# Optimization experiments

Hardware: AMD Instinct MI355X
Metric: run time of the kernel (lower is better)

## Reference

```python
import jax, jax.numpy as jnp
import numpy as np

DIM = 1024
HEADS = 16
HEAD_DIM = DIM // HEADS
EPS = 1e-5


def layer_norm(x, w, b):
    # normalize over last dim (head_dim)
    mu = jnp.mean(x, axis=-1, keepdims=True)
    var = jnp.mean(jnp.square(x - mu), axis=-1, keepdims=True)
    return (x - mu) * jax.lax.rsqrt(var + EPS) * w + b


def setup_inputs() -> dict:
    key = jax.random.key(0)
    ks = jax.random.split(key, 8)
    B, N = 2, 2048
    x = jax.random.normal(ks[0], (B, N, DIM), dtype=jnp.float32)
    mask = jax.random.randint(ks[1], (B, 1, N, N), 0, 2) == 1  # True = masked out
    qkv_w = jax.random.normal(ks[2], (3 * DIM, DIM), dtype=jnp.float32) * (DIM ** -0.5)
    q_norm_w = jnp.ones((HEAD_DIM,), dtype=jnp.float32)
    q_norm_b = jnp.zeros((HEAD_DIM,), dtype=jnp.float32)
    k_norm_w = jnp.ones((HEAD_DIM,), dtype=jnp.float32)
    k_norm_b = jnp.zeros((HEAD_DIM,), dtype=jnp.float32)
    proj_w = jax.random.normal(ks[3], (DIM, DIM), dtype=jnp.float32) * (DIM ** -0.5)
    proj_b = jnp.zeros((DIM,), dtype=jnp.float32)
    return {"x": x, "mask": mask, "qkv_w": qkv_w,
            "q_norm_w": q_norm_w, "q_norm_b": q_norm_b,
            "k_norm_w": k_norm_w, "k_norm_b": k_norm_b,
            "proj_w": proj_w, "proj_b": proj_b}


def reference(x, mask, qkv_w, q_norm_w, q_norm_b, k_norm_w, k_norm_b, proj_w, proj_b):
    B, N, C = x.shape
    H, D = HEADS, HEAD_DIM
    scale = D ** -0.5
    # qkv projection (no bias), split into q,k,v of shape (B,H,N,D)
    qkv = (x @ qkv_w.T).reshape(B, N, 3, H, D).transpose(2, 0, 3, 1, 4)
    q, k, v = qkv[0], qkv[1], qkv[2]
    q = layer_norm(q, q_norm_w, q_norm_b)
    k = layer_norm(k, k_norm_w, k_norm_b)
    q = q * scale
    attn = jnp.einsum("bhnd,bhmd->bhnm", q, k)  # (B,H,N,N)
    attn = jnp.where(mask, -jnp.inf, attn)
    attn = jax.nn.softmax(attn, axis=-1)
    out = jnp.einsum("bhnm,bhmd->bhnd", attn, v)
    out = out.transpose(0, 2, 1, 3).reshape(B, N, C)
    return out @ proj_w.T + proj_b
```

## Files before the change

### kernel.cpp

```cpp
#include <hip/hip_runtime.h>
#include <hip/hip_bf16.h>
#include <math.h>

#define B_    2
#define N_    2048
#define DIM_  1024
#define H_    16
#define HD_   64
#define EPS_  1e-5f
#define SCALE_ 0.125f
#define LOG2E_ 1.4426950408889634f
#define MFIX_  14.0f

typedef __attribute__((ext_vector_type(8))) __bf16 bf16x8;
typedef __attribute__((ext_vector_type(8))) unsigned short ushort8;
typedef __attribute__((ext_vector_type(4))) float f32x4;
typedef __attribute__((ext_vector_type(4))) unsigned int uint4v;

__device__ __forceinline__ unsigned short f2bf(float x) {
    unsigned u = __builtin_bit_cast(unsigned, x);
    u += 0x7fff + ((u >> 16) & 1);
    return (unsigned short)(u >> 16);
}
__device__ __forceinline__ unsigned pk2bf(float a, float b) {
    unsigned ua = __builtin_bit_cast(unsigned, a) + 0x8000u;
    unsigned ub = __builtin_bit_cast(unsigned, b) + 0x8000u;
    return __builtin_amdgcn_perm(ub, ua, 0x07060302);
}

__device__ __forceinline__ void gl_lds16(const void* g, void* l) {
    __builtin_amdgcn_global_load_lds(
        (const __attribute__((address_space(1))) void*)g,
        (__attribute__((address_space(3))) void*)l, 16, 0, 0);
}

__global__ __launch_bounds__(256) void cast_all_bf16(
    const float* __restrict__ x, const float* __restrict__ qkvw,
    const float* __restrict__ pw, unsigned short* __restrict__ out) {
    int i = (blockIdx.x * 256 + threadIdx.x) * 8;
    const float* src;
    if (i < 4194304) src = x + i;
    else if (i < 7340032) src = qkvw + (i - 4194304);
    else src = pw + (i - 7340032);
    float4 v0 = *(const float4*)src;
    float4 v1 = *(const float4*)(src + 4);
    ushort8 r;
    r[0] = f2bf(v0.x); r[1] = f2bf(v0.y); r[2] = f2bf(v0.z); r[3] = f2bf(v0.w);
    r[4] = f2bf(v1.x); r[5] = f2bf(v1.y); r[6] = f2bf(v1.z); r[7] = f2bf(v1.w);
    *(ushort8*)(out + i) = r;
}

__global__ __launch_bounds__(256) void pack_mask(
    const int* __restrict__ mask, unsigned long long* __restrict__ bm) {
    int w = blockIdx.x * 4 + (threadIdx.x >> 6);
    int lane = threadIdx.x & 63;
    int mv = mask[(size_t)w * 64 + lane];
    unsigned long long bits = __ballot(mv != 0);
    if (lane == 0) bm[w] = bits;
}

__global__ __launch_bounds__(256) void gemm_qkv_ln(
    const unsigned short* __restrict__ A, const unsigned short* __restrict__ Bw,
    const float* __restrict__ qnw, const float* __restrict__ qnb,
    const float* __restrict__ knw, const float* __restrict__ knb,
    unsigned short* __restrict__ qbuf, unsigned short* __restrict__ kbuf,
    unsigned short* __restrict__ vbuf) {
    const int K = DIM_;
    __shared__ unsigned short As[128 * 32];
    __shared__ unsigned short Bs[128 * 32];
    const int tid = threadIdx.x;
    const int wave = tid >> 6, lane = tid & 63;
    const int quad = lane >> 4, lcol = lane & 15;
    const int wr = wave >> 1, wc = wave & 1;
    const int row0 = blockIdx.y * 128, col0 = blockIdx.x * 128;

    f32x4 acc[4][4];
#pragma unroll
    for (int i = 0; i < 4; ++i)
#pragma unroll
        for (int j = 0; j < 4; ++j) acc[i][j] = (f32x4){0.f, 0.f, 0.f, 0.f};

    for (int k0 = 0; k0 < K; k0 += 32) {
        __syncthreads();
#pragma unroll
        for (int c = 0; c < 2; ++c) {
            int base = wave * 2048 + c * 1024;
            int myofs = base + lane * 16;
            int r = myofs >> 6;
            int kb = myofs & 63;
            gl_lds16((const char*)A + ((size_t)(row0 + r) * K + k0) * 2 + kb,
                     (char*)As + base);
            gl_lds16((const char*)Bw + ((size_t)(col0 + r) * K + k0) * 2 + kb,
                     (char*)Bs + base);
        }
        __syncthreads();

        bf16x8 af[4], bfr[4];
#pragma unroll
        for (int i = 0; i < 4; ++i) {
            af[i] = *(const bf16x8*)&As[(wr * 64 + i * 16 + lcol) * 32 + quad * 8];
            bfr[i] = *(const bf16x8*)&Bs[(wc * 64 + i * 16 + lcol) * 32 + quad * 8];
        }
#pragma unroll
        for (int i = 0; i < 4; ++i)
#pragma unroll
            for (int j = 0; j < 4; ++j)
                acc[i][j] = __builtin_amdgcn_mfma_f32_16x16x32_bf16(
                    af[i], bfr[j], acc[i][j], 0, 0, 0);
    }

    const int colbase = col0 + wc * 64;
    const int t = colbase >> 10;
    const int h = (colbase & 1023) >> 6;

    if (t < 2) {
        const float* wv = (t == 0) ? qnw : knw;
        const float* bv = (t == 0) ? qnb : knb;
        float wreg[4], breg[4];
#pragma unroll
        for (int j = 0; j < 4; ++j) {
            wreg[j] = wv[j * 16 + lcol];
            breg[j] = bv[j * 16 + lcol];
        }
        const float sc = (t == 0) ? (SCALE_ * LOG2E_) : 1.f;
        unsigned short* obase = (t == 0) ? qbuf : kbuf;
#pragma unroll
        for (int i = 0; i < 4; ++i) {
#pragma unroll
            for (int reg = 0; reg < 4; ++reg) {
                int row = row0 + wr * 64 + i * 16 + quad * 4 + reg;
                int bb = row >> 11, n = row & (N_ - 1);
                float v[4];
#pragma unroll
                for (int j = 0; j < 4; ++j) v[j] = acc[i][j][reg];
                float s = v[0] + v[1] + v[2] + v[3];
                s += __shfl_xor(s, 1);
                s += __shfl_xor(s, 2);
                s += __shfl_xor(s, 4);
                s += __shfl_xor(s, 8);
                float mu = s * (1.f / 64.f);
                float d[4], s2 = 0.f;
#pragma unroll
                for (int j = 0; j < 4; ++j) {
                    d[j] = v[j] - mu;
                    s2 += d[j] * d[j];
                }
                s2 += __shfl_xor(s2, 1);
                s2 += __shfl_xor(s2, 2);
                s2 += __shfl_xor(s2, 4);
                s2 += __shfl_xor(s2, 8);
                float r = rsqrtf(s2 * (1.f / 64.f) + EPS_);
                unsigned short* dst =
                    obase + ((size_t)(bb * H_ + h) * N_ + n) * 64 + lcol;
#pragma unroll
                for (int j = 0; j < 4; ++j)
                    dst[j * 16] = f2bf((d[j] * r * wreg[j] + breg[j]) * sc);
            }
        }
    } else {
        const int dcol = colbase & 1023;
#pragma unroll
        for (int i = 0; i < 4; ++i) {
#pragma unroll
            for (int reg = 0; reg < 4; ++reg) {
                int row = row0 + wr * 64 + i * 16 + quad * 4 + reg;
                unsigned short* dst = vbuf + (size_t)row * DIM_ + dcol + lcol;
#pragma unroll
                for (int j = 0; j < 4; ++j)
                    dst[j * 16] = f2bf(acc[i][j][reg]);
            }
        }
    }
}

template <int WITH_BIAS, int OUT_BF16>
__global__ __launch_bounds__(256) void gemm_bt_mfma(
    const unsigned short* __restrict__ A, const unsigned short* __restrict__ Bw,
    const float* __restrict__ bias, void* __restrict__ Cout, int M, int Ncols,
    int K) {
    __shared__ unsigned short As[128 * 32];
    __shared__ unsigned short Bs[128 * 32];
    const int tid = threadIdx.x;
    const int wave = tid >> 6, lane = tid & 63;
    const int quad = lane >> 4, lcol = lane & 15;
    const int wr = wave >> 1, wc = wave & 1;
    const int row0 = blockIdx.y * 128, col0 = blockIdx.x * 128;

    f32x4 acc[4][4];
#pragma unroll
    for (int i = 0; i < 4; ++i)
#pragma unroll
        for (int j = 0; j < 4; ++j) acc[i][j] = (f32x4){0.f, 0.f, 0.f, 0.f};

    for (int k0 = 0; k0 < K; k0 += 32) {
        __syncthreads();
#pragma unroll
        for (int c = 0; c < 2; ++c) {
            int base = wave * 2048 + c * 1024;
            int myofs = base + lane * 16;
            int r = myofs >> 6;
            int kb = myofs & 63;
            gl_lds16((const char*)A + ((size_t)(row0 + r) * K + k0) * 2 + kb,
                     (char*)As + base);
            gl_lds16((const char*)Bw + ((size_t)(col0 + r) * K + k0) * 2 + kb,
                     (char*)Bs + base);
        }
        __syncthreads();

        bf16x8 af[4], bfr[4];
#pragma unroll
        for (int i = 0; i < 4; ++i) {
            af[i] = *(const bf16x8*)&As[(wr * 64 + i * 16 + lcol) * 32 + quad * 8];
            bfr[i] = *(const bf16x8*)&Bs[(wc * 64 + i * 16 + lcol) * 32 + quad * 8];
        }
#pragma unroll
        for (int i = 0; i < 4; ++i)
#pragma unroll
            for (int j = 0; j < 4; ++j)
                acc[i][j] = __builtin_amdgcn_mfma_f32_16x16x32_bf16(
                    af[i], bfr[j], acc[i][j], 0, 0, 0);
    }

#pragma unroll
    for (int i = 0; i < 4; ++i) {
#pragma unroll
        for (int j = 0; j < 4; ++j) {
            int col = col0 + wc * 64 + j * 16 + lcol;
            float bv = WITH_BIAS ? bias[col] : 0.f;
#pragma unroll
            for (int reg = 0; reg < 4; ++reg) {
                int row = row0 + wr * 64 + i * 16 + quad * 4 + reg;
                float v = acc[i][j][reg] + bv;
                if (OUT_BF16)
                    ((unsigned short*)Cout)[(size_t)row * Ncols + col] = f2bf(v);
                else
                    ((float*)Cout)[(size_t)row * Ncols + col] = v;
            }
        }
    }
}

__global__ __launch_bounds__(256) void transpose_v(
    const unsigned short* __restrict__ vbuf, unsigned short* __restrict__ vt) {
    __shared__ unsigned short Ts[64 * 65];
    const int tid = threadIdx.x;
    const int bh = blockIdx.y, n0 = blockIdx.x * 64;
    const int b = bh >> 4, h = bh & 15;
    {
        int r = tid >> 2, s = tid & 3;
        const unsigned short* src =
            vbuf + (size_t)(b * N_ + n0 + r) * DIM_ + h * 64 + s * 16;
#pragma unroll
        for (int i = 0; i < 16; ++i) Ts[r * 65 + s * 16 + i] = src[i];
    }
    __syncthreads();
    {
        int d = tid >> 2, kt = tid & 3;
        unsigned short* dstrow = vt + (size_t)(bh * 64 + d) * N_ + n0;
        int P = kt >> 1, t = kt & 1;
#pragma unroll
        for (int q = 0; q < 4; ++q) {
            __align__(8) unsigned short tmp4[4];
#pragma unroll
            for (int j = 0; j < 4; ++j)
                tmp4[j] = Ts[(kt * 16 + q * 4 + j) * 65 + d];
            *(uint2*)(dstrow + P * 32 + q * 8 + t * 4) = *(const uint2*)tmp4;
        }
    }
}

__global__ __launch_bounds__(256) void flash_attn_mfma6(
    const unsigned short* __restrict__ q, const unsigned short* __restrict__ k,
    const unsigned short* __restrict__ vt,
    const unsigned long long* __restrict__ bm, unsigned short* __restrict__ ao) {
    __shared__ unsigned short Qs[64 * 64];
    __shared__ unsigned short Ks[2][64 * 64];
    __shared__ unsigned short Vts[2][64 * 64];

    const int tid = threadIdx.x;
    const int wave = tid >> 6, lane = tid & 63;
    const int quad = lane >> 4, lcol = lane & 15;
    const int bh = blockIdx.y, b = bh >> 4, h = bh & 15;
    const int q0 = blockIdx.x * 64;

    const char* kgbase = (const char*)k + (size_t)bh * N_ * 128;
    const char* vtbase = (const char*)vt + (size_t)bh * 64 * N_ * 2;

    const char* kp[2];
    const char* vp[2];
#pragma unroll
    for (int ci = 0; ci < 2; ++ci) {
        int c = wave * 2 + ci;
        int swz = (c & 3) * 2;
        kp[ci] = kgbase + (size_t)(lane ^ swz) * 128 + c * 16;
        vp[ci] = vtbase + (size_t)(lane ^ swz) * N_ * 2 + c * 16;
    }

    {
        const char* qg = (const char*)(q + (size_t)(bh * N_ + q0) * 64);
#pragma unroll
        for (int c = 0; c < 2; ++c) {
            int base = wave * 2048 + c * 1024;
            gl_lds16(qg + base + lane * 16, (char*)Qs + base);
        }
#pragma unroll
        for (int ci = 0; ci < 2; ++ci) {
            int c = wave * 2 + ci;
            gl_lds16(kp[ci], (char*)Ks[0] + c * 1024);
            gl_lds16(vp[ci], (char*)Vts[0] + c * 1024);
            kp[ci] += 64 * 128;
            vp[ci] += 64 * 2;
        }
    }
    const unsigned long long* bmq =
        bm + ((size_t)b * N_ + q0 + wave * 16 + lcol) * 32;
    unsigned long long mw_next = bmq[0];
    __syncthreads();

    bf16x8 bq[2];
#pragma unroll
    for (int d0 = 0; d0 < 2; ++d0)
        bq[d0] = *(const bf16x8*)&Qs[(wave * 16 + lcol) * 64 + d0 * 32 + quad * 8];

    ushort8 ot;
#pragma unroll
    for (int i = 0; i < 8; ++i) ot[i] = 0x3F80;
    const bf16x8 ones = __builtin_bit_cast(bf16x8, ot);

    f32x4 oacc[4];
#pragma unroll
    for (int dt = 0; dt < 4; ++dt) oacc[dt] = (f32x4){0.f, 0.f, 0.f, 0.f};
    f32x4 lacc = (f32x4){0.f, 0.f, 0.f, 0.f};

    for (int k0 = 0; k0 < N_; k0 += 64) {
        const int cur = (k0 >> 6) & 1;
        const unsigned long long mw = mw_next;
        if (k0 + 64 < N_) {
#pragma unroll
            for (int ci = 0; ci < 2; ++ci) {
                int c = wave * 2 + ci;
                gl_lds16(kp[ci], (char*)Ks[cur ^ 1] + c * 1024);
                gl_lds16(vp[ci], (char*)Vts[cur ^ 1] + c * 1024);
                kp[ci] += 64 * 128;
                vp[ci] += 64 * 2;
            }
            mw_next = bmq[(k0 >> 6) + 1];
        }

        unsigned long long mq = mw >> (quad * 4);
        unsigned mlo = (unsigned)mq, mhi = (unsigned)(mq >> 32);
        f32x4 sacc[4];
#pragma unroll
        for (int kt = 0; kt < 4; ++kt) {
            unsigned word = (kt < 2) ? mlo : mhi;
            const int sh = (kt & 1) * 16;
#pragma unroll
            for (int reg = 0; reg < 4; ++reg)
                sacc[kt][reg] = ((word >> (sh + reg)) & 1u) ? -1e4f : -MFIX_;
        }

        const char* ksb = (const char*)Ks[cur];
        const char* vsb = (const char*)Vts[cur];
#pragma unroll
        for (int kt = 0; kt < 4; ++kt) {
#pragma unroll
            for (int d0 = 0; d0 < 2; ++d0) {
                int p = d0 * 4 + quad;
                bf16x8 ak = *(const bf16x8*)(ksb + p * 1024 +
                                             (((kt * 16 + lcol) ^ (quad * 2)) << 4));
                sacc[kt] = __builtin_amdgcn_mfma_f32_16x16x32_bf16(
                    ak, bq[d0], sacc[kt], 0, 0, 0);
            }
        }

        uint2 pk[4];
#pragma unroll
        for (int kt = 0; kt < 4; ++kt) {
            float p0 = exp2f(sacc[kt][0]);
            float p1 = exp2f(sacc[kt][1]);
            float p2 = exp2f(sacc[kt][2]);
            float p3 = exp2f(sacc[kt][3]);
            pk[kt].x = pk2bf(p0, p1);
            pk[kt].y = pk2bf(p2, p3);
        }

#pragma unroll
        for (int P = 0; P < 2; ++P) {
            uint4v bu;
            bu[0] = pk[2 * P].x;
            bu[1] = pk[2 * P].y;
            bu[2] = pk[2 * P + 1].x;
            bu[3] = pk[2 * P + 1].y;
            bf16x8 bp = __builtin_bit_cast(bf16x8, bu);
            lacc = __builtin_amdgcn_mfma_f32_16x16x32_bf16(ones, bp, lacc,
                                                           0, 0, 0);
#pragma unroll
            for (int dt = 0; dt < 4; ++dt) {
                int c = P * 4 + quad;
                bf16x8 va = *(const bf16x8*)(vsb + c * 1024 +
                                             (((dt * 16 + lcol) ^ (quad * 2)) << 4));
                oacc[dt] = __builtin_amdgcn_mfma_f32_16x16x32_bf16(
                    va, bp, oacc[dt], 0, 0, 0);
            }
        }
        __syncthreads();
    }

    float inv = 1.f / lacc[0];
    int row = q0 + wave * 16 + lcol;
    unsigned short* dst = ao + ((size_t)(b * N_ + row)) * DIM_ + h * 64 + quad * 4;
#pragma unroll
    for (int dt = 0; dt < 4; ++dt) {
        uint2 pko;
        pko.x = pk2bf(oacc[dt][0] * inv, oacc[dt][1] * inv);
        pko.y = pk2bf(oacc[dt][2] * inv, oacc[dt][3] * inv);
        *(uint2*)(dst + dt * 16) = pko;
    }
}

extern "C" void kernel_launch(void* const* d_in, const int* in_sizes, int n_in,
                              void* d_out, int out_size, void* d_ws,
                              size_t ws_size, hipStream_t stream) {
    const float* x     = (const float*)d_in[0];
    const int*   mask  = (const int*)d_in[1];
    const float* qkv_w = (const float*)d_in[2];
    const float* qnw   = (const float*)d_in[3];
    const float* qnb   = (const float*)d_in[4];
    const float* knw   = (const float*)d_in[5];
    const float* knb   = (const float*)d_in[6];
    const float* pw    = (const float*)d_in[7];
    const float* pb    = (const float*)d_in[8];
    float* out = (float*)d_out;

    char* ws = (char*)d_ws;
    unsigned short* x_bf  = (unsigned short*)(ws + 0);
    unsigned short* qw_bf = (unsigned short*)(ws + 8388608);
    unsigned short* pw_bf = (unsigned short*)(ws + 14680064);
    unsigned short* qbuf  = (unsigned short*)(ws + 16777216);
    unsigned short* kbuf  = (unsigned short*)(ws + 25165824);
    unsigned short* vbuf  = (unsigned short*)(ws + 33554432);
    unsigned short* vt    = (unsigned short*)(ws + 41943040);
    unsigned long long* bmask = (unsigned long long*)(ws + 50331648);
    unsigned short* ao_bnc = vbuf;

    cast_all_bf16<<<8388608 / 2048, 256, 0, stream>>>(x, qkv_w, pw, x_bf);

    gemm_qkv_ln<<<dim3(3072 / 128, 4096 / 128), 256, 0, stream>>>(
        x_bf, qw_bf, qnw, qnb, knw, knb, qbuf, kbuf, vbuf);

    transpose_v<<<dim3(N_ / 64, B_ * H_), 256, 0, stream>>>(vbuf, vt);

    pack_mask<<<(B_ * N_ * (N_ / 64)) / 4, 256, 0, stream>>>(mask, bmask);

    flash_attn_mfma6<<<dim3(N_ / 64, B_ * H_), 256, 0, stream>>>(
        qbuf, kbuf, vt, bmask, ao_bnc);

    gemm_bt_mfma<1, 0><<<dim3(DIM_ / 128, 4096 / 128), 256, 0, stream>>>(
        ao_bnc, pw_bf, pb, out, B_ * N_, DIM_, DIM_);
}
```

Measured before the change: 293.5 us.

## Vectorize QKV epilogue stores with packed bf16 and shrink proj GEMM tile

The QKV+LayerNorm epilogue now packs four bf16 values per lane into one 8-byte store instead of four scattered 2-byte stores. This permutes the head-dim order within each row, so the V transpose kernel undoes the permutation when it loads. Q and K keep the permuted order, which is harmless because their dot products are order-invariant. The output projection becomes a dedicated kernel with a 128x64 tile that doubles the block count for better CU occupancy, at the cost of less reuse per block.

```diff
diff --git a/kernel.cpp b/kernel.cpp
--- a/kernel.cpp
+++ b/kernel.cpp
@@ -150,71 +150,79 @@
                 s2 += __shfl_xor(s2, 4);
                 s2 += __shfl_xor(s2, 8);
                 float r = rsqrtf(s2 * (1.f / 64.f) + EPS_);
-                unsigned short* dst =
-                    obase + ((size_t)(bb * H_ + h) * N_ + n) * 64 + lcol;
-#pragma unroll
-                for (int j = 0; j < 4; ++j)
-                    dst[j * 16] = f2bf((d[j] * r * wreg[j] + breg[j]) * sc);
+                float o0 = (d[0] * r * wreg[0] + breg[0]) * sc;
+                float o1 = (d[1] * r * wreg[1] + breg[1]) * sc;
+                float o2 = (d[2] * r * wreg[2] + breg[2]) * sc;
+                float o3 = (d[3] * r * wreg[3] + breg[3]) * sc;
+                uint2 pk;
+                pk.x = pk2bf(o0, o1);
+                pk.y = pk2bf(o2, o3);
+                *(uint2*)(obase + ((size_t)(bb * H_ + h) * N_ + n) * 64 +
+                          lcol * 4) = pk;
             }
         }
     } else {
-        const int dcol = colbase & 1023;
 #pragma unroll
         for (int i = 0; i < 4; ++i) {
 #pragma unroll
             for (int reg = 0; reg < 4; ++reg) {
                 int row = row0 + wr * 64 + i * 16 + quad * 4 + reg;
-                unsigned short* dst = vbuf + (size_t)row * DIM_ + dcol + lcol;
-#pragma unroll
-                for (int j = 0; j < 4; ++j)
-                    dst[j * 16] = f2bf(acc[i][j][reg]);
-            }
-        }
-    }
-}
-
-template <int WITH_BIAS, int OUT_BF16>
-__global__ __launch_bounds__(256) void gemm_bt_mfma(
+                uint2 pk;
+                pk.x = pk2bf(acc[i][0][reg], acc[i][1][reg]);
+                pk.y = pk2bf(acc[i][2][reg], acc[i][3][reg]);
+                *(uint2*)(vbuf + (size_t)row * DIM_ + h * 64 + lcol * 4) = pk;
+            }
+        }
+    }
+}
+
+__global__ __launch_bounds__(256) void gemm_proj(
     const unsigned short* __restrict__ A, const unsigned short* __restrict__ Bw,
-    const float* __restrict__ bias, void* __restrict__ Cout, int M, int Ncols,
-    int K) {
+    const float* __restrict__ bias, float* __restrict__ Cout) {
+    const int K = DIM_;
     __shared__ unsigned short As[128 * 32];
-    __shared__ unsigned short Bs[128 * 32];
+    __shared__ unsigned short Bs[64 * 32];
     const int tid = threadIdx.x;
     const int wave = tid >> 6, lane = tid & 63;
     const int quad = lane >> 4, lcol = lane & 15;
-    const int wr = wave >> 1, wc = wave & 1;
-    const int row0 = blockIdx.y * 128, col0 = blockIdx.x * 128;
-
-    f32x4 acc[4][4];
-#pragma unroll
-    for (int i = 0; i < 4; ++i)
+    const int row0 = blockIdx.y * 128, col0 = blockIdx.x * 64;
+
+    f32x4 acc[2][4];
+#pragma unroll
+    for (int i = 0; i < 2; ++i)
 #pragma unroll
         for (int j = 0; j < 4; ++j) acc[i][j] = (f32x4){0.f, 0.f, 0.f, 0.f};
 
     for (int k0 = 0; k0 < K; k0 += 32) {
         __syncthreads();
 #pragma unroll
-        for (int c = 0; c < 2; ++c) {
-            int base = wave * 2048 + c * 1024;
-            int myofs = base + lane * 16;
-            int r = myofs >> 6;
-            int kb = myofs & 63;
-            gl_lds16((const char*)A + ((size_t)(row0 + r) * K + k0) * 2 + kb,
-                     (char*)As + base);
-            gl_lds16((const char*)Bw + ((size_t)(col0 + r) * K + k0) * 2 + kb,
-                     (char*)Bs + base);
+        for (int pi = 0; pi < 3; ++pi) {
+            int p = wave * 3 + pi;
+            if (p < 8) {
+                int base = p * 1024;
+                int myofs = base + lane * 16;
+                int r = myofs >> 6, kb = myofs & 63;
+                gl_lds16((const char*)A + ((size_t)(row0 + r) * K + k0) * 2 + kb,
+                         (char*)As + base);
+            } else {
+                int base = (p - 8) * 1024;
+                int myofs = base + lane * 16;
+                int r = myofs >> 6, kb = myofs & 63;
+                gl_lds16((const char*)Bw + ((size_t)(col0 + r) * K + k0) * 2 + kb,
+                         (char*)Bs + base);
+            }
         }
         __syncthreads();
 
-        bf16x8 af[4], bfr[4];
-#pragma unroll
-        for (int i = 0; i < 4; ++i) {
-            af[i] = *(const bf16x8*)&As[(wr * 64 + i * 16 + lcol) * 32 + quad * 8];
-            bfr[i] = *(const bf16x8*)&Bs[(wc * 64 + i * 16 + lcol) * 32 + quad * 8];
-        }
-#pragma unroll
-        for (int i = 0; i < 4; ++i)
+        bf16x8 af[2], bfr[4];
+#pragma unroll
+        for (int i = 0; i < 2; ++i)
+            af[i] = *(const bf16x8*)&As[(wave * 32 + i * 16 + lcol) * 32 + quad * 8];
+#pragma unroll
+        for (int j = 0; j < 4; ++j)
+            bfr[j] = *(const bf16x8*)&Bs[(j * 16 + lcol) * 32 + quad * 8];
+#pragma unroll
+        for (int i = 0; i < 2; ++i)
 #pragma unroll
             for (int j = 0; j < 4; ++j)
                 acc[i][j] = __builtin_amdgcn_mfma_f32_16x16x32_bf16(
@@ -222,19 +230,15 @@
     }
 
 #pragma unroll
-    for (int i = 0; i < 4; ++i) {
+    for (int i = 0; i < 2; ++i) {
 #pragma unroll
         for (int j = 0; j < 4; ++j) {
-            int col = col0 + wc * 64 + j * 16 + lcol;
-            float bv = WITH_BIAS ? bias[col] : 0.f;
+            int col = col0 + j * 16 + lcol;
+            float bv = bias[col];
 #pragma unroll
             for (int reg = 0; reg < 4; ++reg) {
-                int row = row0 + wr * 64 + i * 16 + quad * 4 + reg;
-                float v = acc[i][j][reg] + bv;
-                if (OUT_BF16)
-                    ((unsigned short*)Cout)[(size_t)row * Ncols + col] = f2bf(v);
-                else
-                    ((float*)Cout)[(size_t)row * Ncols + col] = v;
+                int row = row0 + wave * 32 + i * 16 + quad * 4 + reg;
+                Cout[(size_t)row * DIM_ + col] = acc[i][j][reg] + bv;
             }
         }
     }
@@ -251,7 +255,11 @@
         const unsigned short* src =
             vbuf + (size_t)(b * N_ + n0 + r) * DIM_ + h * 64 + s * 16;
 #pragma unroll
-        for (int i = 0; i < 16; ++i) Ts[r * 65 + s * 16 + i] = src[i];
+        for (int i = 0; i < 16; ++i) {
+            int p = s * 16 + i;
+            int trued = (p >> 2) + (p & 3) * 16;
+            Ts[r * 65 + trued] = src[i];
+        }
     }
     __syncthreads();
     {
@@ -455,6 +463,6 @@
     flash_attn_mfma6<<<dim3(N_ / 64, B_ * H_), 256, 0, stream>>>(
         qbuf, kbuf, vt, bmask, ao_bnc);
 
-    gemm_bt_mfma<1, 0><<<dim3(DIM_ / 128, 4096 / 128), 256, 0, stream>>>(
-        ao_bnc, pw_bf, pb, out, B_ * N_, DIM_, DIM_);
-}
+    gemm_proj<<<dim3(DIM_ / 64, 4096 / 128), 256, 0, stream>>>(
+        ao_bnc, pw_bf, pb, out);
+}
```

Result: no change. 292.1 us (-0.5%).
